# Kernel optimization log

Measured on AMD Instinct MI355X. Metric: run time of the kernel, lower is better.

The kernel has to match this reference:

```python
import jax, jax.numpy as jnp
import numpy as np

F = 32        # num_fields
V = 1000      # per-field vocab (field_dims[i])
D = 64        # embed_dim
B = 8192      # batch
P = F * (F - 1) // 2   # 496 pairs
IN = F * D + P          # 2544 MLP input dim
H1, H2, OUT = 1024, 512, 1000


def setup_inputs() -> dict:
    key = jax.random.key(0)
    ks = jax.random.split(key, 8)
    x = jax.random.randint(ks[0], (B, F), 0, V)
    emb_tables = jax.random.normal(ks[1], (F, V, D), dtype=jnp.float32) * 0.05
    W1 = jax.random.normal(ks[2], (IN, H1), dtype=jnp.float32) * (1.0 / np.sqrt(IN))
    b1 = jnp.zeros((H1,), dtype=jnp.float32)
    W2 = jax.random.normal(ks[3], (H1, H2), dtype=jnp.float32) * (1.0 / np.sqrt(H1))
    b2 = jnp.zeros((H2,), dtype=jnp.float32)
    W3 = jax.random.normal(ks[4], (H2, OUT), dtype=jnp.float32) * (1.0 / np.sqrt(H2))
    b3 = jnp.zeros((OUT,), dtype=jnp.float32)
    return {"x": x, "emb_tables": emb_tables, "W1": W1, "b1": b1,
            "W2": W2, "b2": b2, "W3": W3, "b3": b3}


def reference(x, emb_tables, W1, b1, W2, b2, W3, b3):
    # Per-field embedding lookup: e[b, f] = emb_tables[f, x[b, f]]  -> (B, F, D)
    e = emb_tables[jnp.arange(F)[None, :], x]
    # All pairwise inner products via one batched gram matrix, then triu gather
    gram = jnp.einsum('bid,bjd->bij', e, e)            # (B, F, F)
    iu, ju = jnp.triu_indices(F, k=1)
    cross = gram[:, iu, ju]                             # (B, P)
    h = jnp.concatenate([e.reshape(B, F * D), cross], axis=1)  # (B, IN)
    # MLP (dropout is identity in eval mode)
    h = jax.nn.relu(h @ W1 + b1)
    h = jax.nn.relu(h @ W2 + b2)
    logits = h @ W3 + b3
    return jax.nn.sigmoid(logits)
```

## Files before the change

### kernel.cpp

```cpp
#include <hip/hip_runtime.h>
#include <hip/hip_bf16.h>
#include <cmath>

#define F_   32
#define V_   1000
#define D_   64
#define B_   8192
#define IN_RAW  2544
#define IN_PAD  2560
#define H1_  1024
#define H2_  512
#define OUT_RAW 1000
#define OUT_PAD 1024

typedef __attribute__((ext_vector_type(4))) float f32x4;
typedef __attribute__((ext_vector_type(8))) __bf16 bf16x8;

typedef const __attribute__((address_space(1))) void* gptr_t;
typedef __attribute__((address_space(3))) void* lptr_t;

__device__ __forceinline__ void gload_lds16(const void* g, void* l) {
  __builtin_amdgcn_global_load_lds((gptr_t)g, (lptr_t)l, 16, 0, 0);
}

__global__ __launch_bounds__(256)
void interact_kernel(const int* __restrict__ x, const float* __restrict__ emb,
                     __hip_bfloat16* __restrict__ h)
{
  __shared__ __align__(16) __hip_bfloat16 e4[4][32 * 64];
  const int wid  = threadIdx.x >> 6;
  const int lane = threadIdx.x & 63;
  const int b = blockIdx.x * 4 + wid;
  const int* xb = x + b * F_;
  const size_t hrow = (size_t)b * IN_PAD;

#pragma unroll
  for (int it = 0; it < 8; ++it) {
    const int r = it * 4 + (lane >> 4);
    const int d = (lane & 15) * 4;
    const int idx = xb[r];
    const float4 v = *reinterpret_cast<const float4*>(
        &emb[((size_t)r * V_ + idx) * D_ + d]);
    __hip_bfloat16 t[4];
    t[0] = __float2bfloat16(v.x); t[1] = __float2bfloat16(v.y);
    t[2] = __float2bfloat16(v.z); t[3] = __float2bfloat16(v.w);
    const ushort4 pk = *reinterpret_cast<const ushort4*>(t);
    *reinterpret_cast<ushort4*>(&h[hrow + r * 64 + d]) = pk;
    const int ch = (d >> 3) ^ (r & 7);
    *reinterpret_cast<ushort4*>(&e4[wid][r * 64 + ch * 8 + (d & 7)]) = pk;
  }
  __syncthreads();

  f32x4 g[2][2] = {};
#pragma unroll
  for (int kk = 0; kk < 2; ++kk) {
    bf16x8 fa[2];
#pragma unroll
    for (int t = 0; t < 2; ++t) {
      const int r = t * 16 + (lane & 15);
      const int ch = (kk * 4 + (lane >> 4)) ^ (r & 7);
      fa[t] = *reinterpret_cast<const bf16x8*>(&e4[wid][r * 64 + ch * 8]);
    }
#pragma unroll
    for (int ti = 0; ti < 2; ++ti)
#pragma unroll
      for (int tj = 0; tj < 2; ++tj)
        g[ti][tj] = __builtin_amdgcn_mfma_f32_16x16x32_bf16(fa[ti], fa[tj], g[ti][tj], 0, 0, 0);
  }

#pragma unroll
  for (int ti = 0; ti < 2; ++ti)
#pragma unroll
    for (int tj = 0; tj < 2; ++tj) {
      const int jj = tj * 16 + (lane & 15);
#pragma unroll
      for (int q = 0; q < 4; ++q) {
        const int i = ti * 16 + (lane >> 4) * 4 + q;
        if (i < jj) {
          const int p = i * 31 - (i * (i - 1)) / 2 + (jj - i - 1);
          h[hrow + 2048 + p] = __float2bfloat16(g[ti][tj][q]);
        }
      }
    }
  if (lane < IN_PAD - IN_RAW) h[hrow + IN_RAW + lane] = __float2bfloat16(0.f);
}

__global__ __launch_bounds__(256)
void convert_transpose(const float* __restrict__ W, __hip_bfloat16* __restrict__ Wt,
                       int K, int N, int Kpad, int Npad)
{
  __shared__ float t[32][33];
  const int k0 = blockIdx.x * 32, n0 = blockIdx.y * 32;
  const int tx = threadIdx.x, ty = threadIdx.y;
#pragma unroll
  for (int i = 0; i < 4; ++i) {
    int r = ty + i * 8;
    int k = k0 + r, n = n0 + tx;
    t[r][tx] = (k < K && n < N) ? W[(size_t)k * N + n] : 0.f;
  }
  __syncthreads();
#pragma unroll
  for (int i = 0; i < 4; ++i) {
    int r = ty + i * 8;
    Wt[(size_t)(n0 + r) * Kpad + (k0 + tx)] = __float2bfloat16(t[tx][r]);
  }
}

template <int EPI>
__global__ __launch_bounds__(256)
void gemm_bt(const __hip_bfloat16* __restrict__ A,
             const __hip_bfloat16* __restrict__ Bt,
             const float* __restrict__ bias,
             void* __restrict__ Cout,
             int M, int N, int K, int Nreal)
{
  __shared__ __align__(16) __hip_bfloat16 lds[2][2][128 * 64];

  const int tid  = threadIdx.x;
  const int wid  = tid >> 6;
  const int lane = tid & 63;
  const int wr = wid >> 1, wc = wid & 1;
  const int lr = lane & 15;
  const int lhi = lane >> 4;
  const long rowBase = (long)blockIdx.x * 128;
  const long colBase = (long)blockIdx.y * 128;

  f32x4 acc[4][4] = {};

  const int srow = tid >> 3;
  const long scol = (long)(((tid & 7) ^ (srow & 7)) * 8);
  const long aBase = (rowBase + srow) * (long)K + scol;
  const long bBase = (colBase + srow) * (long)K + scol;

  const int NT = K >> 6;

  auto STAGE = [&](int buf, int t) {
    const long k0 = (long)t * 64;
    char* la = (char*)&lds[buf][0][0] + wid * 1024;
    char* lb = (char*)&lds[buf][1][0] + wid * 1024;
#pragma unroll
    for (int j = 0; j < 4; ++j) {
      gload_lds16(A  + aBase + (long)j * 32 * K + k0, la + j * 4096);
      gload_lds16(Bt + bBase + (long)j * 32 * K + k0, lb + j * 4096);
    }
  };

  STAGE(0, 0);
  __syncthreads();

  int cur = 0;
  for (int t = 0; t < NT; ++t) {
    if (t + 1 < NT) STAGE(cur ^ 1, t + 1);

    const __hip_bfloat16* la = &lds[cur][0][0];
    const __hip_bfloat16* lb = &lds[cur][1][0];
#pragma unroll
    for (int kk = 0; kk < 2; ++kk) {
      const int ch = ((kk * 4 + lhi) ^ (lane & 7)) * 8;
      bf16x8 af[4], bfv[4];
#pragma unroll
      for (int m = 0; m < 4; ++m)
        af[m] = *reinterpret_cast<const bf16x8*>(&la[(wr * 64 + m * 16 + lr) * 64 + ch]);
#pragma unroll
      for (int n = 0; n < 4; ++n)
        bfv[n] = *reinterpret_cast<const bf16x8*>(&lb[(wc * 64 + n * 16 + lr) * 64 + ch]);
#pragma unroll
      for (int m = 0; m < 4; ++m)
#pragma unroll
        for (int n = 0; n < 4; ++n)
          acc[m][n] = __builtin_amdgcn_mfma_f32_16x16x32_bf16(af[m], bfv[n], acc[m][n], 0, 0, 0);
    }
    __syncthreads();
    cur ^= 1;
  }

#pragma unroll
  for (int m = 0; m < 4; ++m) {
    const long row0 = rowBase + wr * 64 + m * 16 + lhi * 4;
#pragma unroll
    for (int n = 0; n < 4; ++n) {
      const int col = (int)colBase + wc * 64 + n * 16 + lr;
      const float bv = (col < Nreal) ? bias[col] : 0.f;
#pragma unroll
      for (int j = 0; j < 4; ++j) {
        float v = acc[m][n][j] + bv;
        const long row = row0 + j;
        if (EPI == 0) {
          v = fmaxf(v, 0.f);
          ((__hip_bfloat16*)Cout)[row * N + col] = __float2bfloat16(v);
        } else {
          if (col < Nreal)
            ((float*)Cout)[row * Nreal + col] = 1.f / (1.f + expf(-v));
        }
      }
    }
  }
}

extern "C" void kernel_launch(void* const* d_in, const int* in_sizes, int n_in,
                              void* d_out, int out_size, void* d_ws, size_t ws_size,
                              hipStream_t stream)
{
  const int*   x   = (const int*)  d_in[0];
  const float* emb = (const float*)d_in[1];
  const float* W1  = (const float*)d_in[2];
  const float* b1  = (const float*)d_in[3];
  const float* W2  = (const float*)d_in[4];
  const float* b2  = (const float*)d_in[5];
  const float* W3  = (const float*)d_in[6];
  const float* b3  = (const float*)d_in[7];
  float* out = (float*)d_out;

  char* ws = (char*)d_ws;
  size_t off = 0;
  auto alloc = [&](size_t bytes) { size_t o = off; off = (off + bytes + 255) & ~255ULL; return o; };
  __hip_bfloat16* h   = (__hip_bfloat16*)(ws + alloc((size_t)B_ * IN_PAD * 2));
  __hip_bfloat16* w1t = (__hip_bfloat16*)(ws + alloc((size_t)H1_ * IN_PAD * 2));
  __hip_bfloat16* w2t = (__hip_bfloat16*)(ws + alloc((size_t)H2_ * H1_ * 2));
  __hip_bfloat16* w3t = (__hip_bfloat16*)(ws + alloc((size_t)OUT_PAD * H2_ * 2));
  __hip_bfloat16* h1  = (__hip_bfloat16*)(ws + alloc((size_t)B_ * H1_ * 2));
  __hip_bfloat16* h2  = (__hip_bfloat16*)(ws + alloc((size_t)B_ * H2_ * 2));

  dim3 tb(32, 8);
  convert_transpose<<<dim3(IN_PAD / 32, H1_ / 32), tb, 0, stream>>>(W1, w1t, IN_RAW, H1_, IN_PAD, H1_);
  convert_transpose<<<dim3(H1_ / 32, H2_ / 32), tb, 0, stream>>>(W2, w2t, H1_, H2_, H1_, H2_);
  convert_transpose<<<dim3(H2_ / 32, OUT_PAD / 32), tb, 0, stream>>>(W3, w3t, H2_, OUT_RAW, H2_, OUT_PAD);

  interact_kernel<<<B_ / 4, 256, 0, stream>>>(x, emb, h);

  gemm_bt<0><<<dim3(B_ / 128, H1_ / 128), 256, 0, stream>>>(h, w1t, b1, h1, B_, H1_, IN_PAD, H1_);
  gemm_bt<0><<<dim3(B_ / 128, H2_ / 128), 256, 0, stream>>>(h1, w2t, b2, h2, B_, H2_, H1_, H2_);
  gemm_bt<1><<<dim3(B_ / 128, OUT_PAD / 128), 256, 0, stream>>>(h2, w3t, b3, out, B_, OUT_PAD, H2_, OUT_RAW);
}
```

Measured before the change: 192.2 us.

## Fuse prep kernels and add 256x128 triple-buffered phased GEMM for layers 1 and 3

Merges the three weight convert-transpose launches and the embedding/interaction kernel into one prep launch, which removes launch overhead and lets these small jobs share the GPU. Adds a new GEMM for the first and last layers that uses 512 threads and 256x128 tiles. It triple-buffers LDS with direct global-to-LDS loads and splits each K-step into four phases, with barriers and raised priority around the MFMA bursts. It also remaps block IDs so neighbouring blocks share tiles in cache. The cost is more LDS per block (144KB) and more barriers per K-step, and the middle layer keeps the old GEMM.

Result: no change. 191.2 us (-0.6%).

```diff
diff --git a/kernel.cpp b/kernel.cpp
--- a/kernel.cpp
+++ b/kernel.cpp
@@ -23,86 +23,239 @@
   __builtin_amdgcn_global_load_lds((gptr_t)g, (lptr_t)l, 16, 0, 0);
 }
 
+#define MF(a, b, c) __builtin_amdgcn_mfma_f32_16x16x32_bf16((a), (b), (c), 0, 0, 0)
+#define SBAR asm volatile("s_barrier" ::: "memory")
+
 __global__ __launch_bounds__(256)
-void interact_kernel(const int* __restrict__ x, const float* __restrict__ emb,
-                     __hip_bfloat16* __restrict__ h)
+void prep_kernel(const int* __restrict__ x, const float* __restrict__ emb,
+                 const float* __restrict__ W1, const float* __restrict__ W2,
+                 const float* __restrict__ W3,
+                 __hip_bfloat16* __restrict__ h, __hip_bfloat16* __restrict__ w1t,
+                 __hip_bfloat16* __restrict__ w2t, __hip_bfloat16* __restrict__ w3t)
 {
-  __shared__ __align__(16) __hip_bfloat16 e4[4][32 * 64];
-  const int wid  = threadIdx.x >> 6;
-  const int lane = threadIdx.x & 63;
-  const int b = blockIdx.x * 4 + wid;
-  const int* xb = x + b * F_;
-  const size_t hrow = (size_t)b * IN_PAD;
-
-#pragma unroll
-  for (int it = 0; it < 8; ++it) {
-    const int r = it * 4 + (lane >> 4);
-    const int d = (lane & 15) * 4;
-    const int idx = xb[r];
-    const float4 v = *reinterpret_cast<const float4*>(
-        &emb[((size_t)r * V_ + idx) * D_ + d]);
-    __hip_bfloat16 t[4];
-    t[0] = __float2bfloat16(v.x); t[1] = __float2bfloat16(v.y);
-    t[2] = __float2bfloat16(v.z); t[3] = __float2bfloat16(v.w);
-    const ushort4 pk = *reinterpret_cast<const ushort4*>(t);
-    *reinterpret_cast<ushort4*>(&h[hrow + r * 64 + d]) = pk;
-    const int ch = (d >> 3) ^ (r & 7);
-    *reinterpret_cast<ushort4*>(&e4[wid][r * 64 + ch * 8 + (d & 7)]) = pk;
-  }
-  __syncthreads();
-
-  f32x4 g[2][2] = {};
-#pragma unroll
-  for (int kk = 0; kk < 2; ++kk) {
-    bf16x8 fa[2];
-#pragma unroll
-    for (int t = 0; t < 2; ++t) {
-      const int r = t * 16 + (lane & 15);
-      const int ch = (kk * 4 + (lane >> 4)) ^ (r & 7);
-      fa[t] = *reinterpret_cast<const bf16x8*>(&e4[wid][r * 64 + ch * 8]);
-    }
+  __shared__ __align__(16) char smem[16384];
+  const int bid = blockIdx.x;
+  const int tid = threadIdx.x;
+
+  if (bid < 3584) {
+    const float* W; __hip_bfloat16* Wt; int K, N, Kpad, kb, nb;
+    if (bid < 2560)      { W = W1; Wt = w1t; K = IN_RAW; N = H1_;     Kpad = IN_PAD; kb = bid % 80; nb = bid / 80; }
+    else if (bid < 3072) { int r = bid - 2560; W = W2; Wt = w2t; K = H1_; N = H2_;   Kpad = H1_;   kb = r % 32;  nb = r / 32; }
+    else                 { int r = bid - 3072; W = W3; Wt = w3t; K = H2_; N = OUT_RAW; Kpad = H2_; kb = r % 16;  nb = r / 16; }
+    float (*t)[33] = (float(*)[33])smem;
+    const int k0 = kb * 32, n0 = nb * 32;
+    const int tx = tid & 31, ty = tid >> 5;
+#pragma unroll
+    for (int i = 0; i < 4; ++i) {
+      int r = ty + i * 8;
+      int k = k0 + r, n = n0 + tx;
+      t[r][tx] = (k < K && n < N) ? W[(size_t)k * N + n] : 0.f;
+    }
+    __syncthreads();
+#pragma unroll
+    for (int i = 0; i < 4; ++i) {
+      int r = ty + i * 8;
+      Wt[(size_t)(n0 + r) * Kpad + (k0 + tx)] = __float2bfloat16(t[tx][r]);
+    }
+  } else {
+    __hip_bfloat16 (*e4)[2048] = (__hip_bfloat16(*)[2048])smem;
+    const int wid  = tid >> 6;
+    const int lane = tid & 63;
+    const int b = (bid - 3584) * 4 + wid;
+    const int* xb = x + b * F_;
+    const size_t hrow = (size_t)b * IN_PAD;
+
+#pragma unroll
+    for (int it = 0; it < 8; ++it) {
+      const int r = it * 4 + (lane >> 4);
+      const int d = (lane & 15) * 4;
+      const int idx = xb[r];
+      const float4 v = *reinterpret_cast<const float4*>(
+          &emb[((size_t)r * V_ + idx) * D_ + d]);
+      __hip_bfloat16 tb[4];
+      tb[0] = __float2bfloat16(v.x); tb[1] = __float2bfloat16(v.y);
+      tb[2] = __float2bfloat16(v.z); tb[3] = __float2bfloat16(v.w);
+      const ushort4 pk = *reinterpret_cast<const ushort4*>(tb);
+      *reinterpret_cast<ushort4*>(&h[hrow + r * 64 + d]) = pk;
+      const int ch = (d >> 3) ^ (r & 7);
+      *reinterpret_cast<ushort4*>(&e4[wid][r * 64 + ch * 8 + (d & 7)]) = pk;
+    }
+    __syncthreads();
+
+    f32x4 g[2][2] = {};
+#pragma unroll
+    for (int kk = 0; kk < 2; ++kk) {
+      bf16x8 fa[2];
+#pragma unroll
+      for (int t2 = 0; t2 < 2; ++t2) {
+        const int r = t2 * 16 + (lane & 15);
+        const int ch = (kk * 4 + (lane >> 4)) ^ (r & 7);
+        fa[t2] = *reinterpret_cast<const bf16x8*>(&e4[wid][r * 64 + ch * 8]);
+      }
+#pragma unroll
+      for (int ti = 0; ti < 2; ++ti)
+#pragma unroll
+        for (int tj = 0; tj < 2; ++tj)
+          g[ti][tj] = MF(fa[ti], fa[tj], g[ti][tj]);
+    }
+
 #pragma unroll
     for (int ti = 0; ti < 2; ++ti)
 #pragma unroll
-      for (int tj = 0; tj < 2; ++tj)
-        g[ti][tj] = __builtin_amdgcn_mfma_f32_16x16x32_bf16(fa[ti], fa[tj], g[ti][tj], 0, 0, 0);
-  }
-
-#pragma unroll
-  for (int ti = 0; ti < 2; ++ti)
-#pragma unroll
-    for (int tj = 0; tj < 2; ++tj) {
-      const int jj = tj * 16 + (lane & 15);
-#pragma unroll
-      for (int q = 0; q < 4; ++q) {
-        const int i = ti * 16 + (lane >> 4) * 4 + q;
-        if (i < jj) {
-          const int p = i * 31 - (i * (i - 1)) / 2 + (jj - i - 1);
-          h[hrow + 2048 + p] = __float2bfloat16(g[ti][tj][q]);
+      for (int tj = 0; tj < 2; ++tj) {
+        const int jj = tj * 16 + (lane & 15);
+#pragma unroll
+        for (int q = 0; q < 4; ++q) {
+          const int i = ti * 16 + (lane >> 4) * 4 + q;
+          if (i < jj) {
+            const int p = i * 31 - (i * (i - 1)) / 2 + (jj - i - 1);
+            h[hrow + 2048 + p] = __float2bfloat16(g[ti][tj][q]);
+          }
         }
       }
-    }
-  if (lane < IN_PAD - IN_RAW) h[hrow + IN_RAW + lane] = __float2bfloat16(0.f);
-}
-
-__global__ __launch_bounds__(256)
-void convert_transpose(const float* __restrict__ W, __hip_bfloat16* __restrict__ Wt,
-                       int K, int N, int Kpad, int Npad)
+    if (lane < IN_PAD - IN_RAW) h[hrow + IN_RAW + lane] = __float2bfloat16(0.f);
+  }
+}
+
+template <int EPI>
+__global__ __launch_bounds__(512, 2)
+void gemm8ph(const __hip_bfloat16* __restrict__ A,
+             const __hip_bfloat16* __restrict__ Bt,
+             const float* __restrict__ bias,
+             void* __restrict__ Cout,
+             int M, int N, int K, int Nreal)
 {
-  __shared__ float t[32][33];
-  const int k0 = blockIdx.x * 32, n0 = blockIdx.y * 32;
-  const int tx = threadIdx.x, ty = threadIdx.y;
-#pragma unroll
-  for (int i = 0; i < 4; ++i) {
-    int r = ty + i * 8;
-    int k = k0 + r, n = n0 + tx;
-    t[r][tx] = (k < K && n < N) ? W[(size_t)k * N + n] : 0.f;
-  }
-  __syncthreads();
-#pragma unroll
-  for (int i = 0; i < 4; ++i) {
-    int r = ty + i * 8;
-    Wt[(size_t)(n0 + r) * Kpad + (k0 + tx)] = __float2bfloat16(t[tx][r]);
+  __shared__ __align__(16) __hip_bfloat16 lds[3][(256 + 128) * 64];
+
+  const int tid  = threadIdx.x;
+  const int wid  = tid >> 6;
+  const int lane = tid & 63;
+  const int wr = wid >> 1;
+  const int wc = wid & 1;
+  const int lr = lane & 15;
+  const int lhi = lane >> 4;
+  const int l7 = lane & 7;
+
+  const int nCol = N >> 7;
+  const int nblk = gridDim.x;
+  const int swz = (blockIdx.x & 7) * (nblk >> 3) + (blockIdx.x >> 3);
+  const long rowBase = (long)(swz / nCol) * 256;
+  const long colBase = (long)(swz % nCol) * 128;
+
+  const int srow = tid >> 3;
+  const long scol = (long)(((tid & 7) ^ (srow & 7)) * 8);
+  const __hip_bfloat16* Ab = A  + (rowBase + srow) * (long)K + scol;
+  const __hip_bfloat16* Bb = Bt + (colBase + srow) * (long)K + scol;
+  char* ldsb = (char*)&lds[0][0];
+  const int NT = K >> 6;
+
+  f32x4 acc[4][4] = {};
+
+  auto stageA = [&](int buf, int t, int j) {
+    gload_lds16(Ab + ((long)j * 64) * K + (long)t * 64,
+                ldsb + buf * 49152 + j * 8192 + wid * 1024);
+  };
+  auto stageB = [&](int buf, int t, int j) {
+    gload_lds16(Bb + ((long)j * 64) * K + (long)t * 64,
+                ldsb + buf * 49152 + 32768 + j * 8192 + wid * 1024);
+  };
+  auto ldA = [&](int buf, int m, int ks) -> bf16x8 {
+    const int row = wr * 64 + m * 16 + lr;
+    const int c = (ks * 4 + lhi) ^ l7;
+    return *(const bf16x8*)(ldsb + buf * 49152 + row * 128 + c * 16);
+  };
+  auto ldB = [&](int buf, int n, int ks) -> bf16x8 {
+    const int row = wc * 64 + n * 16 + lr;
+    const int c = (ks * 4 + lhi) ^ l7;
+    return *(const bf16x8*)(ldsb + buf * 49152 + 32768 + row * 128 + c * 16);
+  };
+
+#pragma unroll
+  for (int j = 0; j < 4; ++j) stageA(0, 0, j);
+  stageB(0, 0, 0); stageB(0, 0, 1);
+#pragma unroll
+  for (int j = 0; j < 4; ++j) stageA(1, 1, j);
+  stageB(1, 1, 0); stageB(1, 1, 1);
+  asm volatile("s_waitcnt vmcnt(6)" ::: "memory");
+  SBAR;
+
+  bf16x8 bv[4][2];
+
+#define PHASE_MFMA(p)                                                     \
+    __builtin_amdgcn_s_setprio(1);                                        \
+    acc[p][0] = MF(a0, bv[0][0], acc[p][0]);                              \
+    acc[p][0] = MF(a1, bv[0][1], acc[p][0]);                              \
+    acc[p][1] = MF(a0, bv[1][0], acc[p][1]);                              \
+    acc[p][1] = MF(a1, bv[1][1], acc[p][1]);                              \
+    acc[p][2] = MF(a0, bv[2][0], acc[p][2]);                              \
+    acc[p][2] = MF(a1, bv[2][1], acc[p][2]);                              \
+    acc[p][3] = MF(a0, bv[3][0], acc[p][3]);                              \
+    acc[p][3] = MF(a1, bv[3][1], acc[p][3]);                              \
+    __builtin_amdgcn_s_setprio(0);
+
+  for (int t = 0; t < NT; ++t) {
+    const int cur = t % 3;
+    const int nxt = (t + 2) % 3;
+    const bool st = (t + 2) < NT;
+
+    {
+#pragma unroll
+      for (int n = 0; n < 4; ++n) {
+        bv[n][0] = ldB(cur, n, 0);
+        bv[n][1] = ldB(cur, n, 1);
+      }
+      bf16x8 a0 = ldA(cur, 0, 0), a1 = ldA(cur, 0, 1);
+      if (st) { stageA(nxt, t + 2, 0); stageA(nxt, t + 2, 1); }
+      SBAR;
+      PHASE_MFMA(0)
+      SBAR;
+    }
+    {
+      bf16x8 a0 = ldA(cur, 1, 0), a1 = ldA(cur, 1, 1);
+      if (st) { stageA(nxt, t + 2, 2); stageA(nxt, t + 2, 3); }
+      SBAR;
+      PHASE_MFMA(1)
+      SBAR;
+    }
+    {
+      bf16x8 a0 = ldA(cur, 2, 0), a1 = ldA(cur, 2, 1);
+      if (st) { stageB(nxt, t + 2, 0); stageB(nxt, t + 2, 1); }
+      SBAR;
+      PHASE_MFMA(2)
+      SBAR;
+    }
+    {
+      bf16x8 a0 = ldA(cur, 3, 0), a1 = ldA(cur, 3, 1);
+      SBAR;
+      PHASE_MFMA(3)
+    }
+    if (t + 1 < NT) {
+      if (st) asm volatile("s_waitcnt vmcnt(6)" ::: "memory");
+      else    asm volatile("s_waitcnt vmcnt(0)" ::: "memory");
+      SBAR;
+    }
+  }
+#undef PHASE_MFMA
+
+#pragma unroll
+  for (int m = 0; m < 4; ++m) {
+    const long row0 = rowBase + wr * 64 + m * 16 + lhi * 4;
+#pragma unroll
+    for (int n = 0; n < 4; ++n) {
+      const int col = (int)colBase + wc * 64 + n * 16 + lr;
+      const float bvs = (col < Nreal) ? bias[col] : 0.f;
+#pragma unroll
+      for (int j = 0; j < 4; ++j) {
+        float v = acc[m][n][j] + bvs;
+        const long row = row0 + j;
+        if (EPI == 0) {
+          ((__hip_bfloat16*)Cout)[row * N + col] = __float2bfloat16(fmaxf(v, 0.f));
+        } else {
+          if (col < Nreal)
+            ((float*)Cout)[row * Nreal + col] = 1.f / (1.f + expf(-v));
+        }
+      }
+    }
   }
 }
 
@@ -168,7 +321,7 @@
       for (int m = 0; m < 4; ++m)
 #pragma unroll
         for (int n = 0; n < 4; ++n)
-          acc[m][n] = __builtin_amdgcn_mfma_f32_16x16x32_bf16(af[m], bfv[n], acc[m][n], 0, 0, 0);
+          acc[m][n] = MF(af[m], bfv[n], acc[m][n]);
     }
     __syncthreads();
     cur ^= 1;
@@ -221,14 +374,9 @@
   __hip_bfloat16* h1  = (__hip_bfloat16*)(ws + alloc((size_t)B_ * H1_ * 2));
   __hip_bfloat16* h2  = (__hip_bfloat16*)(ws + alloc((size_t)B_ * H2_ * 2));
 
-  dim3 tb(32, 8);
-  convert_transpose<<<dim3(IN_PAD / 32, H1_ / 32), tb, 0, stream>>>(W1, w1t, IN_RAW, H1_, IN_PAD, H1_);
-  convert_transpose<<<dim3(H1_ / 32, H2_ / 32), tb, 0, stream>>>(W2, w2t, H1_, H2_, H1_, H2_);
-  convert_transpose<<<dim3(H2_ / 32, OUT_PAD / 32), tb, 0, stream>>>(W3, w3t, H2_, OUT_RAW, H2_, OUT_PAD);
-
-  interact_kernel<<<B_ / 4, 256, 0, stream>>>(x, emb, h);
-
-  gemm_bt<0><<<dim3(B_ / 128, H1_ / 128), 256, 0, stream>>>(h, w1t, b1, h1, B_, H1_, IN_PAD, H1_);
+  prep_kernel<<<5632, 256, 0, stream>>>(x, emb, W1, W2, W3, h, w1t, w2t, w3t);
+
+  gemm8ph<0><<<(B_ / 256) * (H1_ / 128), 512, 0, stream>>>(h, w1t, b1, h1, B_, H1_, IN_PAD, H1_);
   gemm_bt<0><<<dim3(B_ / 128, H2_ / 128), 256, 0, stream>>>(h1, w2t, b2, h2, B_, H2_, H1_, H2_);
-  gemm_bt<1><<<dim3(B_ / 128, OUT_PAD / 128), 256, 0, stream>>>(h2, w3t, b3, out, B_, OUT_PAD, H2_, OUT_RAW);
-}
+  gemm8ph<1><<<(B_ / 256) * (OUT_PAD / 128), 512, 0, stream>>>(h2, w3t, b3, out, B_, OUT_PAD, H2_, OUT_RAW);
+}
```
